# Kernel tuning notes

Hardware: AMD Instinct MI355X
Metric: run time of the kernel (lower is better)

The kernel has to match this reference:

```python
import jax, jax.numpy as jnp
import numpy as np
from jax import lax

B, C, T, H, W = 4, 64, 80, 36, 64
N = 128   # ntargets
NT = 10   # temporal taps


def setup_inputs() -> dict:
    key = jax.random.key(0)
    ks = jax.random.split(key, 8)
    x = jax.random.normal(ks[0], (B, C, T, H, W), dtype=jnp.float32)
    targets = jnp.ones((1, N), dtype=bool)
    wc = ((0.1 * jax.random.normal(ks[1], (C, N)) / 10 + 1) / C).astype(jnp.float32)
    wx = (-0.4 + 0.8 * jax.random.uniform(ks[2], (N,))).astype(jnp.float32)
    wy = (-0.4 + 0.8 * jax.random.uniform(ks[3], (N,))).astype(jnp.float32)
    wsigmax = (0.5 + 0.1 * jax.random.uniform(ks[4], (N,))).astype(jnp.float32)
    wsigmay = (0.5 + 0.1 * jax.random.uniform(ks[5], (N,))).astype(jnp.float32)
    wt = ((1 + 0.1 * jax.random.normal(ks[6], (NT, N))) / NT).astype(jnp.float32)
    wb = (jax.random.normal(ks[7], (N,)) * 0.05 + 0.6).astype(jnp.float32)
    return {"x": x, "targets": targets, "wc": wc, "wx": wx, "wy": wy,
            "wsigmax": wsigmax, "wsigmay": wsigmay, "wt": wt, "wb": wb}


def reference(x, targets, wc, wx, wy, wsigmax, wsigmay, wt, wb):
    b, c, t, h, w = x.shape
    n = wc.shape[1]
    # spatial grids in [-0.5, 0.5), matching torch.meshgrid(indexing='ij')
    yv = (jnp.arange(h, dtype=jnp.float32) - h / 2 + 0.5) / h
    xv = (jnp.arange(w, dtype=jnp.float32) - w / 2 + 0.5) / w
    ygrid, xgrid = jnp.meshgrid(yv, xv, indexing='ij')  # [h, w]

    # Gaussian soft-pooling weights ws: [h*w, n]
    sx = 0.1 + jax.nn.relu(wsigmax) ** 2
    sy = 0.1 + jax.nn.relu(wsigmay) ** 2
    dx = (xgrid.reshape(-1, 1) - wx[None, :]) ** 2 / (2.0 * sx[None, :])
    dy = (ygrid.reshape(-1, 1) - wy[None, :]) ** 2 / (2.0 * sy[None, :])
    ws = jnp.exp(-dx - dy)
    ws = ws / (0.1 + ws.sum(axis=0, keepdims=True))

    # subnet = identity; flatten (batch, time) -> frames, channels x space
    x2 = x.transpose(0, 2, 1, 3, 4).reshape(b * t, c, h * w)  # [bt, c, s]
    # fused channel mix (wc) + spatial soft-pool (ws): out[f, n]
    R = jnp.einsum('fcs,cn,sn->fn', x2, wc, ws, optimize=True)  # [b*t, n]
    R = R.reshape(b, t, n).transpose(0, 2, 1)  # [b, n, t]

    # grouped temporal conv1d (cross-correlation, VALID), one kernel per target
    kern = wt.T[:, None, :]  # [n, 1, nt]
    out = lax.conv_general_dilated(
        R, kern, window_strides=(1,), padding='VALID',
        dimension_numbers=('NCH', 'OIH', 'NCH'), feature_group_count=n)
    return out + wb[None, :, None]  # [b, n, t - nt + 1]
```

## Files before the change

### kernel.cpp

```cpp
#include <hip/hip_runtime.h>
#include <hip/hip_bf16.h>
#include <stdint.h>

#define B_ 4
#define C_ 64
#define T_ 80
#define H_ 36
#define W_ 64
#define N_ 128
#define NT_ 10
#define S_ (H_*W_)
#define M_ (B_*C_*T_)
#define K_ S_
#define TOUT (T_-NT_+1)

#define BM 32
#define BK 64

using float4v = __attribute__((ext_vector_type(4))) float;
using short8v = __attribute__((ext_vector_type(8))) short;

__device__ __forceinline__ unsigned short f2bf(float f) {
  unsigned int u = __float_as_uint(f);
  u += 0x7fffu + ((u >> 16) & 1u);
  return (unsigned short)(u >> 16);
}

__device__ __forceinline__ unsigned int pkbf(float a, float b) {
  union { __hip_bfloat162 h2; unsigned int u; } cv;
  cv.h2 = __float22bfloat162_rn(make_float2(a, b));
  return cv.u;
}

__device__ __forceinline__ void glds16(const void* g, void* l) {
  __builtin_amdgcn_global_load_lds(
      (const __attribute__((address_space(1))) unsigned int*)g,
      (__attribute__((address_space(3))) unsigned int*)l, 16, 0, 0);
}

__global__ __launch_bounds__(256) void k1_ws(const float* __restrict__ wx,
                                             const float* __restrict__ wy,
                                             const float* __restrict__ wsigx,
                                             const float* __restrict__ wsigy,
                                             unsigned short* __restrict__ Bp) {
  const int n = blockIdx.x;
  const int tid = threadIdx.x;
  const float cx = wx[n], cy = wy[n];
  const float rx = fmaxf(wsigx[n], 0.f);
  const float ry = fmaxf(wsigy[n], 0.f);
  const float i2sx = 0.5f / (0.1f + rx * rx);
  const float i2sy = 0.5f / (0.1f + ry * ry);

  float ev[9];
  float part = 0.f;
#pragma unroll
  for (int i = 0; i < 9; ++i) {
    const int s = tid + i * 256;
    const int h = s >> 6, w = s & 63;
    const float dx = (w - 31.5f) * (1.f / 64.f) - cx;
    const float dy = (h - 17.5f) * (1.f / 36.f) - cy;
    const float e = __expf(-(dx * dx * i2sx + dy * dy * i2sy));
    ev[i] = e;
    part += e;
  }
#pragma unroll
  for (int off = 32; off > 0; off >>= 1) part += __shfl_down(part, off);
  __shared__ float red[4];
  if ((tid & 63) == 0) red[tid >> 6] = part;
  __syncthreads();
  const float inv = 1.f / (0.1f + red[0] + red[1] + red[2] + red[3]);
#pragma unroll
  for (int i = 0; i < 9; ++i) {
    const int s = tid + i * 256;
    Bp[((s >> 3) * N_ + n) * 8 + (s & 7)] = f2bf(ev[i] * inv);
  }
}

__global__ __launch_bounds__(256, 4) void k2_gemm(const float* __restrict__ A,
                                                  const unsigned short* __restrict__ Bp,
                                                  float* __restrict__ Z) {
  __shared__ float4v As[BM * 16];
  __shared__ short8v Bs[8 * N_];
  const int tid = threadIdx.x;
  const int lane = tid & 63;
  const int wv = tid >> 6;
  const int wm = wv & 1;
  const int wn = wv >> 1;
  const int m15 = lane & 15;
  const int q = lane >> 4;
  const int mBase = blockIdx.x * BM;

  float4v acc[4];
#pragma unroll
  for (int i = 0; i < 4; ++i) acc[i] = (float4v)(0.f);

  for (int k0 = 0; k0 < K_; k0 += BK) {
#pragma unroll
    for (int i = 0; i < 2; ++i) {
      const int lam = i * 256 + tid;
      const int r = lam >> 4;
      const int c4 = (lam & 15) ^ (r & 15);
      glds16(A + (size_t)(mBase + r) * K_ + k0 + c4 * 4, &As[lam]);
    }
#pragma unroll
    for (int i = 0; i < 4; ++i) {
      const int lam = i * 256 + tid;
      glds16(Bp + (size_t)k0 * N_ + lam * 8, &Bs[lam]);
    }
    __syncthreads();

#pragma unroll
    for (int ks = 0; ks < 2; ++ks) {
      const int c4a = ks * 8 + q * 2;
      const int rowc = (wm * 16 + m15) * 16;
      const float4v alo = As[rowc + (c4a ^ m15)];
      const float4v ahi = As[rowc + ((c4a + 1) ^ m15)];
      union { short8v s8; unsigned int u[4]; } af;
      af.u[0] = pkbf(alo[0], alo[1]);
      af.u[1] = pkbf(alo[2], alo[3]);
      af.u[2] = pkbf(ahi[0], ahi[1]);
      af.u[3] = pkbf(ahi[2], ahi[3]);
      const int g = ks * 4 + q;
#pragma unroll
      for (int nt = 0; nt < 4; ++nt) {
        const short8v bf = Bs[g * N_ + wn * 64 + nt * 16 + m15];
        acc[nt] = __builtin_amdgcn_mfma_f32_16x16x32_bf16(af.s8, bf, acc[nt], 0, 0, 0);
      }
    }
    __syncthreads();
  }

#pragma unroll
  for (int nt = 0; nt < 4; ++nt) {
#pragma unroll
    for (int v = 0; v < 4; ++v) {
      Z[(size_t)(mBase + wm * 16 + q * 4 + v) * N_ + wn * 64 + nt * 16 + m15] =
          acc[nt][v];
    }
  }
}

__global__ __launch_bounds__(128) void k3_reduce_c(const float* __restrict__ Z,
                                                   const float* __restrict__ wc,
                                                   float* __restrict__ R) {
  const int n = threadIdx.x;
  const int bt = blockIdx.x;
  const int b = bt / T_;
  const int t = bt - b * T_;
  float s = 0.f;
#pragma unroll 8
  for (int c = 0; c < C_; ++c) {
    s += Z[(size_t)((b * C_ + c) * T_ + t) * N_ + n] * wc[c * N_ + n];
  }
  R[(b * T_ + t) * N_ + n] = s;
}

__global__ __launch_bounds__(128) void k4_conv(const float* __restrict__ R,
                                               const float* __restrict__ wt,
                                               const float* __restrict__ wb,
                                               float* __restrict__ out) {
  const int n = threadIdx.x;
  const int tau = blockIdx.x;
  const int b = blockIdx.y;
  float s = wb[n];
#pragma unroll
  for (int j = 0; j < NT_; ++j) {
    s += R[(b * T_ + tau + j) * N_ + n] * wt[j * N_ + n];
  }
  out[((size_t)b * N_ + n) * TOUT + tau] = s;
}

extern "C" void kernel_launch(void* const* d_in, const int* in_sizes, int n_in,
                              void* d_out, int out_size, void* d_ws, size_t ws_size,
                              hipStream_t stream) {
  (void)in_sizes; (void)n_in; (void)out_size; (void)ws_size;
  const float* x    = (const float*)d_in[0];
  const float* wc   = (const float*)d_in[2];
  const float* wx   = (const float*)d_in[3];
  const float* wy   = (const float*)d_in[4];
  const float* wsx  = (const float*)d_in[5];
  const float* wsy  = (const float*)d_in[6];
  const float* wt   = (const float*)d_in[7];
  const float* wb   = (const float*)d_in[8];
  float* out = (float*)d_out;

  char* ws = (char*)d_ws;
  unsigned short* Bp = (unsigned short*)ws;
  float* R = (float*)(ws + 589824);
  float* Z = (float*)(ws + 589824 + 163840);

  k1_ws<<<N_, 256, 0, stream>>>(wx, wy, wsx, wsy, Bp);
  k2_gemm<<<M_ / BM, 256, 0, stream>>>(x, Bp, Z);
  k3_reduce_c<<<B_ * T_, 128, 0, stream>>>(Z, wc, R);
  dim3 g4(TOUT, B_);
  k4_conv<<<g4, 128, 0, stream>>>(R, wt, wb, out);
}
```

Before: 299.0 us.

## Split-K GEMM with double-buffered A tiles and direct B loads from global

The GEMM kernel now splits K in two across a second grid dimension, writing two partial Z buffers that the channel-reduction kernel sums. A tiles are double-buffered in shared memory so the next tile's load overlaps compute, and B fragments are read straight from global/L2 instead of being staged in LDS. Each wave now owns a 32x32 output tile rather than 16x64. The aim is more parallelism and latency hiding on the memory-bound x stream, at the cost of twice the Z traffic and uncached-in-LDS B reads.

Measured after the change: 297.0 us. No clear change (-0.7%).

```diff
diff --git a/kernel.cpp b/kernel.cpp
--- a/kernel.cpp
+++ b/kernel.cpp
@@ -16,6 +16,8 @@
 
 #define BM 32
 #define BK 64
+#define KSPLIT 2
+#define NIT (K_ / (BK * KSPLIT))
 
 using float4v = __attribute__((ext_vector_type(4))) float;
 using short8v = __attribute__((ext_vector_type(8))) short;
@@ -78,79 +80,98 @@
 
 __global__ __launch_bounds__(256, 4) void k2_gemm(const float* __restrict__ A,
                                                   const unsigned short* __restrict__ Bp,
-                                                  float* __restrict__ Z) {
-  __shared__ float4v As[BM * 16];
-  __shared__ short8v Bs[8 * N_];
+                                                  float* __restrict__ Zp) {
+  __shared__ float4v As[2][BM * 16];
   const int tid = threadIdx.x;
   const int lane = tid & 63;
   const int wv = tid >> 6;
-  const int wm = wv & 1;
-  const int wn = wv >> 1;
   const int m15 = lane & 15;
   const int q = lane >> 4;
   const int mBase = blockIdx.x * BM;
-
-  float4v acc[4];
-#pragma unroll
-  for (int i = 0; i < 4; ++i) acc[i] = (float4v)(0.f);
-
-  for (int k0 = 0; k0 < K_; k0 += BK) {
-#pragma unroll
-    for (int i = 0; i < 2; ++i) {
-      const int lam = i * 256 + tid;
-      const int r = lam >> 4;
-      const int c4 = (lam & 15) ^ (r & 15);
-      glds16(A + (size_t)(mBase + r) * K_ + k0 + c4 * 4, &As[lam]);
+  const int split = blockIdx.y;
+  const int kStart = split * (K_ / KSPLIT);
+
+  const float* ga[2];
+  int lam_[2];
+#pragma unroll
+  for (int i = 0; i < 2; ++i) {
+    const int lam = i * 256 + tid;
+    const int r = lam >> 4;
+    const int c4 = (lam & 15) ^ (r & 15);
+    ga[i] = A + (size_t)(mBase + r) * K_ + kStart + c4 * 4;
+    lam_[i] = lam;
+  }
+
+  float4v acc[2][2];
+#pragma unroll
+  for (int i = 0; i < 2; ++i)
+#pragma unroll
+    for (int j = 0; j < 2; ++j) acc[i][j] = (float4v)(0.f);
+
+#pragma unroll
+  for (int i = 0; i < 2; ++i) glds16(ga[i], &As[0][lam_[i]]);
+
+  int cur = 0;
+  for (int it = 0; it < NIT; ++it) {
+    __syncthreads();
+    if (it + 1 < NIT) {
+#pragma unroll
+      for (int i = 0; i < 2; ++i)
+        glds16(ga[i] + (size_t)(it + 1) * BK, &As[cur ^ 1][lam_[i]]);
     }
-#pragma unroll
-    for (int i = 0; i < 4; ++i) {
-      const int lam = i * 256 + tid;
-      glds16(Bp + (size_t)k0 * N_ + lam * 8, &Bs[lam]);
-    }
-    __syncthreads();
-
+    const int kg0 = (kStart + it * BK) >> 3;
 #pragma unroll
     for (int ks = 0; ks < 2; ++ks) {
       const int c4a = ks * 8 + q * 2;
-      const int rowc = (wm * 16 + m15) * 16;
-      const float4v alo = As[rowc + (c4a ^ m15)];
-      const float4v ahi = As[rowc + ((c4a + 1) ^ m15)];
-      union { short8v s8; unsigned int u[4]; } af;
-      af.u[0] = pkbf(alo[0], alo[1]);
-      af.u[1] = pkbf(alo[2], alo[3]);
-      af.u[2] = pkbf(ahi[0], ahi[1]);
-      af.u[3] = pkbf(ahi[2], ahi[3]);
-      const int g = ks * 4 + q;
-#pragma unroll
-      for (int nt = 0; nt < 4; ++nt) {
-        const short8v bf = Bs[g * N_ + wn * 64 + nt * 16 + m15];
-        acc[nt] = __builtin_amdgcn_mfma_f32_16x16x32_bf16(af.s8, bf, acc[nt], 0, 0, 0);
+      union { short8v s8; unsigned int u[4]; } af[2];
+#pragma unroll
+      for (int mt = 0; mt < 2; ++mt) {
+        const int rowc = (mt * 16 + m15) * 16;
+        const float4v alo = As[cur][rowc + (c4a ^ m15)];
+        const float4v ahi = As[cur][rowc + ((c4a + 1) ^ m15)];
+        af[mt].u[0] = pkbf(alo[0], alo[1]);
+        af[mt].u[1] = pkbf(alo[2], alo[3]);
+        af[mt].u[2] = pkbf(ahi[0], ahi[1]);
+        af[mt].u[3] = pkbf(ahi[2], ahi[3]);
+      }
+      const int kg = kg0 + ks * 4 + q;
+#pragma unroll
+      for (int nt = 0; nt < 2; ++nt) {
+        const int col = wv * 32 + nt * 16 + m15;
+        const short8v bf =
+            *(const short8v*)(Bp + ((size_t)kg * N_ + col) * 8);
+        acc[0][nt] = __builtin_amdgcn_mfma_f32_16x16x32_bf16(af[0].s8, bf, acc[0][nt], 0, 0, 0);
+        acc[1][nt] = __builtin_amdgcn_mfma_f32_16x16x32_bf16(af[1].s8, bf, acc[1][nt], 0, 0, 0);
       }
     }
-    __syncthreads();
-  }
-
-#pragma unroll
-  for (int nt = 0; nt < 4; ++nt) {
-#pragma unroll
-    for (int v = 0; v < 4; ++v) {
-      Z[(size_t)(mBase + wm * 16 + q * 4 + v) * N_ + wn * 64 + nt * 16 + m15] =
-          acc[nt][v];
-    }
-  }
-}
-
-__global__ __launch_bounds__(128) void k3_reduce_c(const float* __restrict__ Z,
+    cur ^= 1;
+  }
+
+  float* Z = Zp + (size_t)split * M_ * N_;
+#pragma unroll
+  for (int mt = 0; mt < 2; ++mt)
+#pragma unroll
+    for (int nt = 0; nt < 2; ++nt)
+#pragma unroll
+      for (int v = 0; v < 4; ++v)
+        Z[(size_t)(mBase + mt * 16 + q * 4 + v) * N_ + wv * 32 + nt * 16 + m15] =
+            acc[mt][nt][v];
+}
+
+__global__ __launch_bounds__(128) void k3_reduce_c(const float* __restrict__ Zp,
                                                    const float* __restrict__ wc,
                                                    float* __restrict__ R) {
   const int n = threadIdx.x;
   const int bt = blockIdx.x;
   const int b = bt / T_;
   const int t = bt - b * T_;
+  const float* Z0 = Zp;
+  const float* Z1 = Zp + (size_t)M_ * N_;
   float s = 0.f;
 #pragma unroll 8
   for (int c = 0; c < C_; ++c) {
-    s += Z[(size_t)((b * C_ + c) * T_ + t) * N_ + n] * wc[c * N_ + n];
+    const size_t idx = (size_t)((b * C_ + c) * T_ + t) * N_ + n;
+    s += (Z0[idx] + Z1[idx]) * wc[c * N_ + n];
   }
   R[(b * T_ + t) * N_ + n] = s;
 }
@@ -187,11 +208,12 @@
   char* ws = (char*)d_ws;
   unsigned short* Bp = (unsigned short*)ws;
   float* R = (float*)(ws + 589824);
-  float* Z = (float*)(ws + 589824 + 163840);
+  float* Zp = (float*)(ws + 589824 + 163840);
 
   k1_ws<<<N_, 256, 0, stream>>>(wx, wy, wsx, wsy, Bp);
-  k2_gemm<<<M_ / BM, 256, 0, stream>>>(x, Bp, Z);
-  k3_reduce_c<<<B_ * T_, 128, 0, stream>>>(Z, wc, R);
+  dim3 g2(M_ / BM, KSPLIT);
+  k2_gemm<<<g2, 256, 0, stream>>>(x, Bp, Zp);
+  k3_reduce_c<<<B_ * T_, 128, 0, stream>>>(Zp, wc, R);
   dim3 g4(TOUT, B_);
   k4_conv<<<g4, 128, 0, stream>>>(R, wt, wb, out);
 }
```
